# Kernel optimization log

Hardware: AMD Instinct MI355X
Metric: run time of the kernel (lower is better)

The kernel has to match this reference:

```python
import jax, jax.numpy as jnp
import numpy as np

DIM = 768
HEADS = 12
DIM_HEAD = 64
INNER = HEADS * DIM_HEAD  # 768
B, N = 8, 1024


def layernorm(x, gamma, beta, eps=1e-5):
    mu = jnp.mean(x, axis=-1, keepdims=True)
    var = jnp.var(x, axis=-1, keepdims=True)
    return (x - mu) * jax.lax.rsqrt(var + eps) * gamma + beta


def setup_inputs() -> dict:
    key = jax.random.key(0)
    ks = jax.random.split(key, 12)
    s = lambda fan_in: 1.0 / np.sqrt(fan_in)
    return {
        "x": jax.random.normal(ks[0], (B, N, DIM), dtype=jnp.float32),
        "ln1_g": jnp.ones((DIM,), jnp.float32),
        "ln1_b": jnp.zeros((DIM,), jnp.float32),
        "ln2_g": jnp.ones((DIM,), jnp.float32),
        "ln2_b": jnp.zeros((DIM,), jnp.float32),
        "w_qkv": jax.random.uniform(ks[1], (DIM, 3 * INNER), jnp.float32, -s(DIM), s(DIM)),
        "w_out": jax.random.uniform(ks[2], (INNER, DIM), jnp.float32, -s(INNER), s(INNER)),
        "b_out": jax.random.uniform(ks[3], (DIM,), jnp.float32, -s(INNER), s(INNER)),
        "w_ff1": jax.random.uniform(ks[4], (DIM, 4 * DIM), jnp.float32, -s(DIM), s(DIM)),
        "b_ff1": jax.random.uniform(ks[5], (4 * DIM,), jnp.float32, -s(DIM), s(DIM)),
        "w_ff2": jax.random.uniform(ks[6], (4 * DIM, DIM), jnp.float32, -s(4 * DIM), s(4 * DIM)),
        "b_ff2": jax.random.uniform(ks[7], (DIM,), jnp.float32, -s(4 * DIM), s(4 * DIM)),
    }


def reference(x, ln1_g, ln1_b, ln2_g, ln2_b, w_qkv, w_out, b_out, w_ff1, b_ff1, w_ff2, b_ff2):
    # --- attention sub-block (dropout = identity, eval mode) ---
    residual = x
    h = layernorm(x, ln1_g, ln1_b)
    qkv = h @ w_qkv  # [B, N, 3*INNER]
    q, k, v = jnp.split(qkv, 3, axis=-1)
    # b n (h d) -> b h n d
    reshape = lambda t: t.reshape(B, N, HEADS, DIM_HEAD).transpose(0, 2, 1, 3)
    q, k, v = reshape(q), reshape(k), reshape(v)
    scale = DIM_HEAD ** -0.5
    attn = jnp.einsum('bhnd,bhmd->bhnm', q, k) * scale
    attn = jax.nn.softmax(attn, axis=-1)
    out = jnp.einsum('bhnm,bhmd->bhnd', attn, v)
    out = out.transpose(0, 2, 1, 3).reshape(B, N, INNER)  # b h n d -> b n (h d)
    out = out @ w_out + b_out
    x = residual + out
    # --- FFN sub-block ---
    h2 = layernorm(x, ln2_g, ln2_b)
    ff = jax.nn.gelu(h2 @ w_ff1 + b_ff1, approximate=False) @ w_ff2 + b_ff2
    return x + ff
```

## Files before the change

kernel.cpp:

```cpp
#include <hip/hip_runtime.h>
#include <hip/hip_bf16.h>
#include <math.h>
#include <stdint.h>

#define BATCH 8
#define SEQ   1024
#define DIM   768
#define HEADS 12
#define DHEAD 64
#define TOK   (BATCH*SEQ)
#define INNER 768
#define FFDIM 3072
#define QKVN  2304
#define QKLD  1536

typedef float floatx4 __attribute__((ext_vector_type(4)));
typedef __bf16 bf16x8 __attribute__((ext_vector_type(8)));

__device__ __forceinline__ float b2f(uint16_t u) {
    return __uint_as_float(((uint32_t)u) << 16);
}
__device__ __forceinline__ uint16_t f2b(float f) {
    uint32_t x = __float_as_uint(f);
    x += 0x7fffu + ((x >> 16) & 1u);
    return (uint16_t)(x >> 16);
}
__device__ __forceinline__ uint32_t cvt_pk_bf16(float lo, float hi) {
    uint32_t r;
    asm("v_cvt_pk_bf16_f32 %0, %1, %2" : "=v"(r) : "v"(lo), "v"(hi));
    return r;
}
__device__ __forceinline__ float exp2_fast(float x) {
    float r; asm("v_exp_f32 %0, %1" : "=v"(r) : "v"(x)); return r;
}
__device__ __forceinline__ float rcp_fast(float x) {
    float r; asm("v_rcp_f32 %0, %1" : "=v"(r) : "v"(x)); return r;
}

__device__ __forceinline__ float gelu_exact(float v) {
    float x  = v * 0.70710678f;
    float ax = fabsf(x);
    float t  = rcp_fast(fmaf(0.3275911f, ax, 1.0f));
    float poly = t * fmaf(t, fmaf(t, fmaf(t, fmaf(t, 1.061405429f, -1.453152027f),
                          1.421413741f), -0.284496736f), 0.254829592f);
    float e = 1.0f - poly * exp2_fast(x * x * -1.44269504f);
    float erfv = copysignf(e, x);
    return 0.5f * v * (1.0f + erfv);
}

__device__ __forceinline__ void gload_lds16(const uint16_t* g, uint16_t* l) {
    __builtin_amdgcn_global_load_lds(
        (const __attribute__((address_space(1))) uint32_t*)g,
        (__attribute__((address_space(3))) uint32_t*)l, 16, 0, 0);
}

__global__ __launch_bounds__(256) void transpose_convert(
    const float* __restrict__ in, uint16_t* __restrict__ outT, int R, int C)
{
    __shared__ float tile[32][33];
    int c0 = blockIdx.x * 32, r0 = blockIdx.y * 32;
    int x = threadIdx.x;
    int y = threadIdx.y;
    #pragma unroll
    for (int i = y; i < 32; i += 8)
        tile[i][x] = in[(size_t)(r0 + i) * C + c0 + x];
    __syncthreads();
    #pragma unroll
    for (int i = y; i < 32; i += 8)
        outT[(size_t)(c0 + i) * R + r0 + x] = f2b(tile[x][i]);
}

__global__ __launch_bounds__(64) void ln_naive(
    const float* __restrict__ x, const float* __restrict__ g,
    const float* __restrict__ be, uint16_t* __restrict__ y)
{
    const int lane = threadIdx.x;
    const size_t row = blockIdx.x;
    float v[12];
    float s = 0.f, ss = 0.f;
    #pragma unroll
    for (int j = 0; j < 12; j++) {
        int idx = lane + j * 64;
        float f = x[row * DIM + idx];
        v[j] = f; s += f; ss += f * f;
    }
    #pragma unroll
    for (int off = 32; off > 0; off >>= 1) {
        s  += __shfl_xor(s, off);
        ss += __shfl_xor(ss, off);
    }
    const float mu = s * (1.f / DIM);
    const float var = ss * (1.f / DIM) - mu * mu;
    const float rstd = rsqrtf(var + 1e-5f);
    #pragma unroll
    for (int j = 0; j < 12; j++) {
        int idx = lane + j * 64;
        y[row * DIM + idx] = f2b((v[j] - mu) * rstd * g[idx] + be[idx]);
    }
}

#define GEMM_STAGE(buf, kk) do {                                                            \
    _Pragma("unroll")                                                                       \
    for (int i = 0; i < 2; i++) {                                                           \
        int row = i * 64 + srow;                                                            \
        gload_lds16(A  + (size_t)(tileM + row) * lda  + (kk) + scol, &a_tile[buf][row * 32 + scol]); \
        gload_lds16(Bt + (size_t)(tileN + row) * ldbt + (kk) + scol, &b_tile[buf][row * 32 + scol]); \
    } } while (0)

template<bool BIAS, bool GELU, bool RES, bool OUTF, bool VSPLIT>
__global__ __launch_bounds__(256) void gemm_bt(
    const uint16_t* __restrict__ A, const uint16_t* __restrict__ Bt,
    void* C, const float* __restrict__ bias, int bias_off,
    const float* res, int N, int K, int lda, int ldbt, int ldc,
    uint16_t* __restrict__ vt)
{
    __shared__ __align__(16) uint16_t a_tile[2][128 * 32];
    __shared__ __align__(16) uint16_t b_tile[2][128 * 32];
    const int tid = threadIdx.x;
    const int wave = tid >> 6, lane = tid & 63;
    const int wr = wave >> 1, wc = wave & 1;

    const int nwg = gridDim.x * gridDim.y;
    int bid = blockIdx.y * gridDim.x + blockIdx.x;
    if ((nwg & 7) == 0)
        bid = (bid & 7) * (nwg >> 3) + (bid >> 3);
    const int tileM = (bid / gridDim.x) * 128;
    const int tileN = (bid % gridDim.x) * 128;

    floatx4 acc[4][4] = {};

    const int scol = (tid & 3) * 8;
    const int srow = tid >> 2;
    const int lm = lane & 15;
    const int lq = lane >> 4;
    const int kq = lq * 8;

    GEMM_STAGE(0, 0);
    asm volatile("s_waitcnt vmcnt(0)" ::: "memory");
    __syncthreads();

    int cur = 0;
    for (int k0 = 0; k0 < K; k0 += 32) {
        if (k0 + 32 < K) GEMM_STAGE(cur ^ 1, k0 + 32);

        bf16x8 af[4], bfr[4];
        #pragma unroll
        for (int rt = 0; rt < 4; rt++) {
            int r = wr * 64 + rt * 16 + lm;
            af[rt] = *(const bf16x8*)&a_tile[cur][r * 32 + kq];
        }
        #pragma unroll
        for (int nt = 0; nt < 4; nt++) {
            int n = wc * 64 + nt * 16 + lm;
            bfr[nt] = *(const bf16x8*)&b_tile[cur][n * 32 + kq];
        }
        #pragma unroll
        for (int rt = 0; rt < 4; rt++)
            #pragma unroll
            for (int nt = 0; nt < 4; nt++)
                acc[rt][nt] = __builtin_amdgcn_mfma_f32_16x16x32_bf16(
                    af[rt], bfr[nt], acc[rt][nt], 0, 0, 0);

        __syncthreads();
        cur ^= 1;
    }

    const bool vpath = VSPLIT && (tileN >= 1536);
    #pragma unroll
    for (int rt = 0; rt < 4; rt++) {
        int r0 = tileM + wr * 64 + rt * 16 + lq * 4;
        #pragma unroll
        for (int nt = 0; nt < 4; nt++) {
            int cg = tileN + wc * 64 + nt * 16 + lm;
            if (vpath) {
                int d = cg - 1536;
                int bb = r0 >> 10, s0 = r0 & 1023;
                uint32_t p0 = (uint32_t)f2b(acc[rt][nt][0]) | ((uint32_t)f2b(acc[rt][nt][1]) << 16);
                uint32_t p1 = (uint32_t)f2b(acc[rt][nt][2]) | ((uint32_t)f2b(acc[rt][nt][3]) << 16);
                uint2 pk; pk.x = p0; pk.y = p1;
                *(uint2*)&vt[((size_t)bb * 768 + d) * 1024 + s0] = pk;
            } else {
                float bvv = BIAS ? bias[bias_off + cg] : 0.f;
                #pragma unroll
                for (int r = 0; r < 4; r++) {
                    float v = acc[rt][nt][r] + bvv;
                    if (GELU) v = gelu_exact(v);
                    size_t ci = (size_t)(r0 + r) * ldc + cg;
                    if (RES) v += res[ci];
                    if (OUTF) ((float*)C)[ci] = v;
                    else      ((uint16_t*)C)[ci] = f2b(v);
                }
            }
        }
    }
}

#define KSWZ(row, cb) ((cb) ^ (((row) & 7) << 4))
#define NKT (SEQ / 64)
#define SM_C   0.18033688f
#define SM_THR 11.5416f

__global__ __launch_bounds__(256) void flash_mfma(
    uint16_t* qk, const uint16_t* __restrict__ vt)
{
    __shared__ __align__(16) uint16_t k_s[2][64 * 64];
    __shared__ __align__(16) uint16_t v_s[2][64 * 64];
    __shared__ __align__(16) uint16_t p_s[64 * 64];
    char* k_base = (char*)k_s;
    char* v_base = (char*)v_s;
    char* p_c    = (char*)p_s;

    const int t = threadIdx.x;
    const int wq = t >> 6;
    const int lane = t & 63;
    const int lm = lane & 15;
    const int lq = lane >> 4;

    int flat = blockIdx.x + 16 * (blockIdx.y + 12 * blockIdx.z);
    int nw = (flat & 7) * 192 + (flat >> 3);
    const int b  = nw / 192;
    const int rem = nw - b * 192;
    const int h  = rem >> 4;
    const int qb = rem & 15;

    const size_t rowbase = (size_t)b * SEQ;
    const int hcol = h * DHEAD;

    bf16x8 qf[2];
    {
        const uint16_t* qp = qk + (rowbase + qb*64 + wq*16 + lm) * QKLD + hcol + lq*8;
        qf[0] = *(const bf16x8*)qp;
        qf[1] = *(const bf16x8*)(qp + 32);
    }

    floatx4 O[4] = {};
    float m_q = -1e30f, l_q = 0.f;

    const int s_row = t >> 2;
    const int s_cb  = (t & 3) * 32;
    const size_t kgbase = (rowbase + s_row) * QKLD + INNER + hcol;
    const size_t vgbase = ((size_t)b * 768 + hcol + s_row) * 1024;

    uint4 kr0, kr1, vr0, vr1;
    {
        const char* kp = (const char*)(qk + kgbase);
        kr0 = *(const uint4*)(kp + s_cb);
        kr1 = *(const uint4*)(kp + s_cb + 16);
        const char* vp = (const char*)(vt + vgbase);
        vr0 = *(const uint4*)(vp + s_cb);
        vr1 = *(const uint4*)(vp + s_cb + 16);
        *(uint4*)&k_base[s_row*128 + KSWZ(s_row, s_cb)]      = kr0;
        *(uint4*)&k_base[s_row*128 + KSWZ(s_row, s_cb + 16)] = kr1;
        *(uint4*)&v_base[s_row*128 + KSWZ(s_row, s_cb)]      = vr0;
        *(uint4*)&v_base[s_row*128 + KSWZ(s_row, s_cb + 16)] = vr1;
    }

    int cur = 0;
    for (int kt = 0; kt < NKT; ++kt) {
        __syncthreads();

        if (kt + 1 < NKT) {
            const char* kp = (const char*)(qk + kgbase + (size_t)(kt + 1) * 64 * QKLD);
            kr0 = *(const uint4*)(kp + s_cb);
            kr1 = *(const uint4*)(kp + s_cb + 16);
            const char* vp = (const char*)(vt + vgbase + (size_t)(kt + 1) * 64);
            vr0 = *(const uint4*)(vp + s_cb);
            vr1 = *(const uint4*)(vp + s_cb + 16);
        }

        const char* k_c = k_base + cur * 8192;
        const char* v_c = v_base + cur * 8192;

        floatx4 S[4];
        #pragma unroll
        for (int nt = 0; nt < 4; nt++) {
            const int row = nt*16 + lm;
            bf16x8 ak0 = *(const bf16x8*)&k_c[row*128 + KSWZ(row, lq*16)];
            bf16x8 ak1 = *(const bf16x8*)&k_c[row*128 + KSWZ(row, 64 + lq*16)];
            floatx4 a = {};
            a = __builtin_amdgcn_mfma_f32_16x16x32_bf16(ak0, qf[0], a, 0, 0, 0);
            a = __builtin_amdgcn_mfma_f32_16x16x32_bf16(ak1, qf[1], a, 0, 0, 0);
            S[nt] = a;
        }

        float m0 = fmaxf(fmaxf(S[0][0], S[0][1]), fmaxf(S[0][2], S[0][3]));
        float m1 = fmaxf(fmaxf(S[1][0], S[1][1]), fmaxf(S[1][2], S[1][3]));
        float m2 = fmaxf(fmaxf(S[2][0], S[2][1]), fmaxf(S[2][2], S[2][3]));
        float m3 = fmaxf(fmaxf(S[3][0], S[3][1]), fmaxf(S[3][2], S[3][3]));
        float mx = fmaxf(fmaxf(m0, m1), fmaxf(m2, m3)) * SM_C;
        mx = fmaxf(mx, __shfl_xor(mx, 16));
        mx = fmaxf(mx, __shfl_xor(mx, 32));

        float mn = m_q;
        if (!__all(mx <= m_q + SM_THR)) {
            mn = fmaxf(m_q, mx);
            float alpha = exp2_fast(m_q - mn);
            m_q = mn;
            l_q *= alpha;
            #pragma unroll
            for (int nt = 0; nt < 4; nt++) {
                O[nt][0] *= alpha; O[nt][1] *= alpha;
                O[nt][2] *= alpha; O[nt][3] *= alpha;
            }
        }

        float p[4][4];
        float sum = 0.f;
        #pragma unroll
        for (int nt = 0; nt < 4; nt++) {
            float p0 = exp2_fast(fmaf(S[nt][0], SM_C, -mn));
            float p1 = exp2_fast(fmaf(S[nt][1], SM_C, -mn));
            float p2 = exp2_fast(fmaf(S[nt][2], SM_C, -mn));
            float p3 = exp2_fast(fmaf(S[nt][3], SM_C, -mn));
            p[nt][0] = p0; p[nt][1] = p1; p[nt][2] = p2; p[nt][3] = p3;
            sum += (p0 + p1) + (p2 + p3);
        }
        sum += __shfl_xor(sum, 16);
        sum += __shfl_xor(sum, 32);
        l_q += sum;

        const int prow = wq*16 + lm;
        #pragma unroll
        for (int nt = 0; nt < 4; nt++) {
            uint2 w;
            w.x = cvt_pk_bf16(p[nt][0], p[nt][1]);
            w.y = cvt_pk_bf16(p[nt][2], p[nt][3]);
            *(uint2*)&p_c[prow*128 + KSWZ(prow, nt*32 + lq*8)] = w;
        }

        #pragma unroll
        for (int ks = 0; ks < 2; ks++) {
            bf16x8 bp = *(const bf16x8*)&p_c[prow*128 + KSWZ(prow, ks*64 + lq*16)];
            #pragma unroll
            for (int nt = 0; nt < 4; nt++) {
                const int vrow = nt*16 + lm;
                bf16x8 av = *(const bf16x8*)&v_c[vrow*128 + KSWZ(vrow, ks*64 + lq*16)];
                O[nt] = __builtin_amdgcn_mfma_f32_16x16x32_bf16(av, bp, O[nt], 0, 0, 0);
            }
        }

        if (kt + 1 < NKT) {
            char* kn = k_base + (cur ^ 1) * 8192;
            char* vn = v_base + (cur ^ 1) * 8192;
            *(uint4*)&kn[s_row*128 + KSWZ(s_row, s_cb)]      = kr0;
            *(uint4*)&kn[s_row*128 + KSWZ(s_row, s_cb + 16)] = kr1;
            *(uint4*)&vn[s_row*128 + KSWZ(s_row, s_cb)]      = vr0;
            *(uint4*)&vn[s_row*128 + KSWZ(s_row, s_cb + 16)] = vr1;
        }
        cur ^= 1;
    }

    const float linv = rcp_fast(l_q);
    uint16_t* dst = qk + (rowbase + qb*64 + wq*16 + lm) * QKLD + hcol;
    #pragma unroll
    for (int nt = 0; nt < 4; nt++) {
        uint2 w;
        w.x = cvt_pk_bf16(O[nt][0] * linv, O[nt][1] * linv);
        w.y = cvt_pk_bf16(O[nt][2] * linv, O[nt][3] * linv);
        *(uint2*)&dst[nt*16 + lq*4] = w;
    }
}

extern "C" void kernel_launch(void* const* d_in, const int* in_sizes, int n_in,
                              void* d_out, int out_size, void* d_ws, size_t ws_size,
                              hipStream_t stream) {
    const float* x      = (const float*)d_in[0];
    const float* ln1_g  = (const float*)d_in[1];
    const float* ln1_b  = (const float*)d_in[2];
    const float* ln2_g  = (const float*)d_in[3];
    const float* ln2_b  = (const float*)d_in[4];
    const float* w_qkv  = (const float*)d_in[5];
    const float* w_out  = (const float*)d_in[6];
    const float* b_out  = (const float*)d_in[7];
    const float* w_ff1  = (const float*)d_in[8];
    const float* b_ff1  = (const float*)d_in[9];
    const float* w_ff2  = (const float*)d_in[10];
    const float* b_ff2  = (const float*)d_in[11];
    float* out = (float*)d_out;

    uint16_t* ws  = (uint16_t*)d_ws;
    uint16_t* qk  = ws;
    uint16_t* ffc = ws;
    uint16_t* vT  = ws + (size_t)12582912;
    uint16_t* h   = ws + (size_t)18874368;
    uint16_t* WqT = ws + (size_t)25165824;
    uint16_t* WoT = ws + (size_t)26935296;
    uint16_t* W1T = ws + (size_t)27525120;
    uint16_t* W2T = ws + (size_t)29884416;

    dim3 tb(32, 8);
    hipLaunchKernelGGL(transpose_convert, dim3(QKVN/32, DIM/32), tb, 0, stream, w_qkv, WqT, DIM, QKVN);
    hipLaunchKernelGGL(transpose_convert, dim3(DIM/32,  DIM/32), tb, 0, stream, w_out, WoT, DIM, DIM);
    hipLaunchKernelGGL(transpose_convert, dim3(FFDIM/32, DIM/32), tb, 0, stream, w_ff1, W1T, DIM, FFDIM);
    hipLaunchKernelGGL(transpose_convert, dim3(DIM/32, FFDIM/32), tb, 0, stream, w_ff2, W2T, FFDIM, DIM);

    hipLaunchKernelGGL(ln_naive, dim3(TOK), dim3(64), 0, stream, x, ln1_g, ln1_b, h);
    hipLaunchKernelGGL((gemm_bt<false, false, false, false, true>), dim3(QKVN/128, TOK/128), dim3(256), 0, stream,
                       h, WqT, qk, nullptr, 0, nullptr, QKVN, DIM, DIM, DIM, QKLD, vT);
    hipLaunchKernelGGL(flash_mfma, dim3(SEQ/64, HEADS, BATCH), dim3(256), 0, stream, qk, vT);
    hipLaunchKernelGGL((gemm_bt<true, false, true, true, false>), dim3(DIM/128, TOK/128), dim3(256), 0, stream,
                       qk, WoT, out, b_out, 0, x, DIM, INNER, QKLD, DIM, DIM, nullptr);
    hipLaunchKernelGGL(ln_naive, dim3(TOK), dim3(64), 0, stream, out, ln2_g, ln2_b, h);
    for (int c = 0; c < 2; c++) {
        hipLaunchKernelGGL((gemm_bt<true, true, false, false, false>), dim3(1536/128, TOK/128), dim3(256), 0, stream,
                           h, W1T + (size_t)c*1536*DIM, ffc, b_ff1, c*1536, nullptr,
                           1536, DIM, DIM, DIM, 1536, nullptr);
        if (c == 0) {
            hipLaunchKernelGGL((gemm_bt<true, false, true, true, false>), dim3(DIM/128, TOK/128), dim3(256), 0, stream,
                               ffc, W2T + (size_t)c*1536, out, b_ff2, 0, out,
                               DIM, 1536, 1536, FFDIM, DIM, nullptr);
        } else {
            hipLaunchKernelGGL((gemm_bt<false, false, true, true, false>), dim3(DIM/128, TOK/128), dim3(256), 0, stream,
                               ffc, W2T + (size_t)c*1536, out, nullptr, 0, out,
                               DIM, 1536, 1536, FFDIM, DIM, nullptr);
        }
    }
}
```

Measured before the change: 432.3 us.

## Triple-buffer GEMM LDS tiles with one barrier per k-step and partial vmcnt waits

Moves the bf16 GEMM main loop from double to triple buffering in LDS, so loads run two k-steps ahead. Each iteration waits only for the oldest stage's loads (vmcnt(4)) and uses a single s_barrier instead of a full vmcnt(0) wait plus a trailing __syncthreads. The aim is to hide global-to-LDS latency behind MFMA work. In exchange LDS use rises to 48KB per block, which may lower occupancy, and correctness now relies on the vmcnt count matching the four loads issued per stage.

```diff
diff --git a/kernel.cpp b/kernel.cpp
--- a/kernel.cpp
+++ b/kernel.cpp
@@ -103,8 +103,8 @@
     _Pragma("unroll")                                                                       \
     for (int i = 0; i < 2; i++) {                                                           \
         int row = i * 64 + srow;                                                            \
-        gload_lds16(A  + (size_t)(tileM + row) * lda  + (kk) + scol, &a_tile[buf][row * 32 + scol]); \
-        gload_lds16(Bt + (size_t)(tileN + row) * ldbt + (kk) + scol, &b_tile[buf][row * 32 + scol]); \
+        gload_lds16(A  + (size_t)(tileM + row) * lda  + (kk) + scol, &a_s[buf][row * 32 + scol]); \
+        gload_lds16(Bt + (size_t)(tileN + row) * ldbt + (kk) + scol, &b_s[buf][row * 32 + scol]); \
     } } while (0)
 
 template<bool BIAS, bool GELU, bool RES, bool OUTF, bool VSPLIT>
@@ -114,8 +114,8 @@
     const float* res, int N, int K, int lda, int ldbt, int ldc,
     uint16_t* __restrict__ vt)
 {
-    __shared__ __align__(16) uint16_t a_tile[2][128 * 32];
-    __shared__ __align__(16) uint16_t b_tile[2][128 * 32];
+    __shared__ __align__(16) uint16_t a_s[3][128 * 32];
+    __shared__ __align__(16) uint16_t b_s[3][128 * 32];
     const int tid = threadIdx.x;
     const int wave = tid >> 6, lane = tid & 63;
     const int wr = wave >> 1, wc = wave & 1;
@@ -135,34 +135,40 @@
     const int lq = lane >> 4;
     const int kq = lq * 8;
 
+    const int nt = K >> 5;
+
     GEMM_STAGE(0, 0);
-    asm volatile("s_waitcnt vmcnt(0)" ::: "memory");
-    __syncthreads();
-
-    int cur = 0;
-    for (int k0 = 0; k0 < K; k0 += 32) {
-        if (k0 + 32 < K) GEMM_STAGE(cur ^ 1, k0 + 32);
+    GEMM_STAGE(1, 32);
+
+    int rd = 0, st = 2;
+    for (int t = 0; t < nt; ++t) {
+        if (t == nt - 1) asm volatile("s_waitcnt vmcnt(0)" ::: "memory");
+        else             asm volatile("s_waitcnt vmcnt(4)" ::: "memory");
+        __builtin_amdgcn_s_barrier();
+        __builtin_amdgcn_sched_barrier(0);
+
+        if (t + 2 < nt) GEMM_STAGE(st, (t + 2) * 32);
 
         bf16x8 af[4], bfr[4];
         #pragma unroll
         for (int rt = 0; rt < 4; rt++) {
             int r = wr * 64 + rt * 16 + lm;
-            af[rt] = *(const bf16x8*)&a_tile[cur][r * 32 + kq];
-        }
-        #pragma unroll
-        for (int nt = 0; nt < 4; nt++) {
-            int n = wc * 64 + nt * 16 + lm;
-            bfr[nt] = *(const bf16x8*)&b_tile[cur][n * 32 + kq];
+            af[rt] = *(const bf16x8*)&a_s[rd][r * 32 + kq];
+        }
+        #pragma unroll
+        for (int ntt = 0; ntt < 4; ntt++) {
+            int n = wc * 64 + ntt * 16 + lm;
+            bfr[ntt] = *(const bf16x8*)&b_s[rd][n * 32 + kq];
         }
         #pragma unroll
         for (int rt = 0; rt < 4; rt++)
             #pragma unroll
-            for (int nt = 0; nt < 4; nt++)
-                acc[rt][nt] = __builtin_amdgcn_mfma_f32_16x16x32_bf16(
-                    af[rt], bfr[nt], acc[rt][nt], 0, 0, 0);
-
-        __syncthreads();
-        cur ^= 1;
+            for (int ntt = 0; ntt < 4; ntt++)
+                acc[rt][ntt] = __builtin_amdgcn_mfma_f32_16x16x32_bf16(
+                    af[rt], bfr[ntt], acc[rt][ntt], 0, 0, 0);
+
+        rd = rd + 1; if (rd == 3) rd = 0;
+        st = st + 1; if (st == 3) st = 0;
     }
 
     const bool vpath = VSPLIT && (tileN >= 1536);
@@ -170,20 +176,20 @@
     for (int rt = 0; rt < 4; rt++) {
         int r0 = tileM + wr * 64 + rt * 16 + lq * 4;
         #pragma unroll
-        for (int nt = 0; nt < 4; nt++) {
-            int cg = tileN + wc * 64 + nt * 16 + lm;
+        for (int ntt = 0; ntt < 4; ntt++) {
+            int cg = tileN + wc * 64 + ntt * 16 + lm;
             if (vpath) {
                 int d = cg - 1536;
                 int bb = r0 >> 10, s0 = r0 & 1023;
-                uint32_t p0 = (uint32_t)f2b(acc[rt][nt][0]) | ((uint32_t)f2b(acc[rt][nt][1]) << 16);
-                uint32_t p1 = (uint32_t)f2b(acc[rt][nt][2]) | ((uint32_t)f2b(acc[rt][nt][3]) << 16);
+                uint32_t p0 = (uint32_t)f2b(acc[rt][ntt][0]) | ((uint32_t)f2b(acc[rt][ntt][1]) << 16);
+                uint32_t p1 = (uint32_t)f2b(acc[rt][ntt][2]) | ((uint32_t)f2b(acc[rt][ntt][3]) << 16);
                 uint2 pk; pk.x = p0; pk.y = p1;
                 *(uint2*)&vt[((size_t)bb * 768 + d) * 1024 + s0] = pk;
             } else {
                 float bvv = BIAS ? bias[bias_off + cg] : 0.f;
                 #pragma unroll
                 for (int r = 0; r < 4; r++) {
-                    float v = acc[rt][nt][r] + bvv;
+                    float v = acc[rt][ntt][r] + bvv;
                     if (GELU) v = gelu_exact(v);
                     size_t ci = (size_t)(r0 + r) * ldc + cg;
                     if (RES) v += res[ci];
```

Result: no change. 424.8 us (-1.7%).
